# Performance work log

Measured on AMD Instinct MI355X. Metric: run time of the kernel, lower is better.

Reference implementation:

```python
import jax, jax.numpy as jnp
import numpy as np

B = 4096
D = 2048
K = 8          # num_intention
H2 = 64        # fc2 out


def setup_inputs() -> dict:
    key = jax.random.key(0)
    ks = jax.random.split(key, 8)
    x = jax.random.normal(ks[0], (B, D), dtype=jnp.float32)
    # one-hot intention per sample
    idx = jax.random.randint(ks[1], (B,), 0, K)
    intention = jax.nn.one_hot(idx, K, dtype=jnp.float32)
    s1 = 1.0 / np.sqrt(D)
    s2 = 1.0 / np.sqrt(K)
    s3 = 1.0 / np.sqrt(D + H2)
    W1 = jax.random.uniform(ks[2], (D * K, D), jnp.float32, -s1, s1)
    b1 = jax.random.uniform(ks[3], (D * K,), jnp.float32, -s1, s1)
    W2 = jax.random.uniform(ks[4], (H2, K), jnp.float32, -s2, s2)
    b2 = jax.random.uniform(ks[5], (H2,), jnp.float32, -s2, s2)
    W3 = jax.random.uniform(ks[6], (1, D + H2), jnp.float32, -s3, s3)
    b3 = jax.random.uniform(ks[7], (1,), jnp.float32, -s3, s3)
    return {"x": x, "intention": intention, "W1": W1, "b1": b1,
            "W2": W2, "b2": b2, "W3": W3, "b3": b3}


def reference(x, intention, W1, b1, W2, b2, W3, b3):
    # fc2 on the one-hot intention -> [B, 64]
    y2 = intention @ W2.T + b2
    # fc1 densely computes all K branches (dropout treated as identity / eval mode)
    y1 = x @ W1.T + b1                      # [B, D*K]
    # mask = intention.repeat(1, 2048): branch axis is INNERMOST (interleaved)
    y1 = y1.reshape(B, D, K)                # [B, D, K]
    sel = jax.lax.stop_gradient(intention)  # mask is non-differentiable in torch
    y1 = jnp.einsum('bdk,bk->bd', y1, sel)  # gather active branch -> [B, D]
    y3 = jax.nn.relu(jnp.concatenate([y1, y2], axis=1))  # [B, D+64]
    y = y3 @ W3.T + b3                      # [B, 1]
    return y
```

## Files before the change

### kernel.cpp

```cpp
#include <hip/hip_runtime.h>
#include <hip/hip_bf16.h>
#include <stdint.h>

#define NB 4096
#define ND 2048
#define NK 8
#define NH 64

#define BM 128
#define BN 128
#define BK 32
#define MAX_ROWS 5120
#define MAX_TILES 40

#define CONV_BLOCKS  (NK * ND)
#define XCONV_BLOCKS NB
#define KIDX_BLOCKS  (NB / 256)
#define PREP_GRID    (CONV_BLOCKS + XCONV_BLOCKS + KIDX_BLOCKS)

typedef __bf16 bf16;
typedef __bf16 bf16x8 __attribute__((ext_vector_type(8)));
typedef float floatx4 __attribute__((ext_vector_type(4)));

#define OFF_KIDX   0u
#define OFF_ORDER  16384u
#define OFF_META   40960u
#define OFF_CUR    41472u
#define OFF_C2S    41536u
#define OFF_CNTP   41600u
#define OFF_XC     65536u
#define OFF_WB     16842752u

__device__ inline void cvt_row16(const float* __restrict__ src, bf16* __restrict__ dst) {
    float4 a = *(const float4*)(src);
    float4 c = *(const float4*)(src + 4);
    bf16x8 v;
    v[0] = (bf16)a.x; v[1] = (bf16)a.y; v[2] = (bf16)a.z; v[3] = (bf16)a.w;
    v[4] = (bf16)c.x; v[5] = (bf16)c.y; v[6] = (bf16)c.z; v[7] = (bf16)c.w;
    *(bf16x8*)dst = v;
}

__global__ void __launch_bounds__(256)
prep_conv_kernel(const float* __restrict__ x,
                 const float* __restrict__ intention,
                 const float* __restrict__ W1,
                 int* __restrict__ kidx,
                 int* __restrict__ cntp,
                 bf16* __restrict__ xc,
                 bf16* __restrict__ Wb)
{
    const int blk = blockIdx.x;
    const int tid = threadIdx.x;

    if (blk < CONV_BLOCKS) {
        const int d = blk >> 3;
        const int k = blk & 7;
        cvt_row16(W1 + (size_t)blk * ND + tid * 8,
                  Wb + ((size_t)k * ND + d) * ND + tid * 8);
    } else if (blk < CONV_BLOCKS + XCONV_BLOCKS) {
        const int row = blk - CONV_BLOCKS;
        cvt_row16(x + (size_t)row * ND + tid * 8,
                  xc + (size_t)row * ND + tid * 8);
    } else {
        __shared__ int h[NK];
        const int hb = blk - CONV_BLOCKS - XCONV_BLOCKS;
        if (tid < NK) h[tid] = 0;
        __syncthreads();
        const int b = hb * 256 + tid;
        float4 a = *(const float4*)(intention + (size_t)b * NK);
        float4 c = *(const float4*)(intention + (size_t)b * NK + 4);
        int k = 0;
        if (a.y > 0.5f) k = 1;
        if (a.z > 0.5f) k = 2;
        if (a.w > 0.5f) k = 3;
        if (c.x > 0.5f) k = 4;
        if (c.y > 0.5f) k = 5;
        if (c.z > 0.5f) k = 6;
        if (c.w > 0.5f) k = 7;
        kidx[b] = k;
        atomicAdd(&h[k], 1);
        __syncthreads();
        if (tid < NK) cntp[hb * NK + tid] = h[tid];
    }
}

__global__ void __launch_bounds__(256)
meta_kernel(const int* __restrict__ cntp,
            const float* __restrict__ W2,
            const float* __restrict__ b2,
            const float* __restrict__ W3,
            const float* __restrict__ b3,
            int* __restrict__ meta,
            int* __restrict__ cursors,
            float* __restrict__ c2s)
{
    __shared__ int cnt[NK];
    const int tid = threadIdx.x;
    if (tid < NK) {
        int s = 0;
#pragma unroll
        for (int i = 0; i < KIDX_BLOCKS; i++) s += cntp[i * NK + tid];
        cnt[tid] = s;
    }
    if (tid >= 64 && tid < 128) {
        const int l = tid - 64;
        const int k = l & 7;
        const int hc = l >> 3;
        float s = 0.f;
#pragma unroll
        for (int j = 0; j < 8; j++) {
            int h = hc * 8 + j;
            float v = W2[h * NK + k] + b2[h];
            if (v > 0.f) s += v * W3[ND + h];
        }
        s += __shfl_xor(s, 8, 64);
        s += __shfl_xor(s, 16, 64);
        s += __shfl_xor(s, 32, 64);
        if (l < 8) c2s[k] = s + b3[0];
    }
    __syncthreads();
    if (tid == 0) {
        int running = 0, nt = 0;
        for (int k = 0; k < NK; k++) {
            cursors[k] = running;
            int ntile = (cnt[k] + BM - 1) / BM;
            for (int t = 0; t < ntile && nt < MAX_TILES; t++) {
                meta[1 + nt] = k;
                meta[1 + MAX_TILES + nt] = running + t * BM;
                nt++;
            }
            running += ntile * BM;
        }
        meta[0] = nt;
    }
}

__global__ void __launch_bounds__(256)
scatter_kernel(const int* __restrict__ kidx,
               int* __restrict__ cursors,
               const float* __restrict__ c2s,
               int* __restrict__ order,
               float* __restrict__ out)
{
    const int b = blockIdx.x * 256 + threadIdx.x;
    const int lane = threadIdx.x & 63;
    const int k = kidx[b] & 7;
    out[b] = c2s[k];

    const unsigned long long below = (lane == 63) ? ~0ull >> 1
                                   : ((1ull << lane) - 1);
    int pos = 0;
#pragma unroll
    for (int kk = 0; kk < NK; kk++) {
        unsigned long long m = __ballot(k == kk);
        if (m) {
            int leader = __ffsll((long long)m) - 1;
            int base = 0;
            if (lane == leader) base = atomicAdd(&cursors[kk], __popcll(m));
            base = __shfl(base, leader, 64);
            if (k == kk) pos = base + __popcll(m & below);
        }
    }
    if (pos >= 0 && pos < MAX_ROWS) order[pos] = b;
}

__global__ void __launch_bounds__(256)
gemm_kernel(const bf16* __restrict__ xc,
            const bf16* __restrict__ Wb,
            const int* __restrict__ order,
            const int* __restrict__ meta,
            const float* __restrict__ b1,
            const float* __restrict__ W3,
            float* __restrict__ out)
{
    int n_mt = meta[0];
    if (n_mt > MAX_TILES) n_mt = MAX_TILES;
    const int mt = blockIdx.y;
    if (mt >= n_mt) return;
    const int kbr = meta[1 + mt] & 7;
    int row0 = meta[1 + MAX_TILES + mt];
    if (row0 < 0) row0 = 0;
    if (row0 > MAX_ROWS - BM) row0 = MAX_ROWS - BM;
    const int col0 = blockIdx.x * BN;

    __shared__ bf16 As[BM * BK];
    __shared__ bf16 Bs[BN * BK];
    __shared__ int rowb[BM];

    const int tid = threadIdx.x;
    const int lane = tid & 63;
    const int wid = tid >> 6;
    const int wm = wid >> 1;
    const int wn = wid & 1;

    if (tid < BM) {
        int b = order[row0 + tid];
        rowb[tid] = (b >= 0 && b < NB) ? b : -1;
    }
    __syncthreads();

    const int srow = tid >> 2;
    const int scol = (tid & 3) * 8;
    const int ra0 = rowb[srow];
    const int ra1 = rowb[64 + srow];
    const bf16* pa0 = xc + (size_t)(ra0 < 0 ? 0 : ra0) * ND + scol;
    const bf16* pa1 = xc + (size_t)(ra1 < 0 ? 0 : ra1) * ND + scol;
    const bf16* pb0 = Wb + ((size_t)kbr * ND + col0 + srow) * ND + scol;
    const bf16* pb1 = pb0 + (size_t)64 * ND;
    bf16* la0 = As + wid * 512;
    bf16* la1 = As + 2048 + wid * 512;
    bf16* lb0 = Bs + wid * 512;
    bf16* lb1 = Bs + 2048 + wid * 512;

    floatx4 zero = {0.f, 0.f, 0.f, 0.f};
    floatx4 acc[4][4];
#pragma unroll
    for (int i = 0; i < 4; i++)
#pragma unroll
        for (int j = 0; j < 4; j++) acc[i][j] = zero;

    const int qk = (lane >> 4) * 8;
    const int mrow = lane & 15;

    for (int kk = 0; kk < ND; kk += BK) {
        __builtin_amdgcn_global_load_lds(
            (const __attribute__((address_space(1))) void*)(pa0 + kk),
            (__attribute__((address_space(3))) void*)la0, 16, 0, 0);
        __builtin_amdgcn_global_load_lds(
            (const __attribute__((address_space(1))) void*)(pa1 + kk),
            (__attribute__((address_space(3))) void*)la1, 16, 0, 0);
        __builtin_amdgcn_global_load_lds(
            (const __attribute__((address_space(1))) void*)(pb0 + kk),
            (__attribute__((address_space(3))) void*)lb0, 16, 0, 0);
        __builtin_amdgcn_global_load_lds(
            (const __attribute__((address_space(1))) void*)(pb1 + kk),
            (__attribute__((address_space(3))) void*)lb1, 16, 0, 0);
        __syncthreads();

        bf16x8 af[4], bfv[4];
#pragma unroll
        for (int i = 0; i < 4; i++) {
            af[i]  = *(const bf16x8*)(As + (wm * 64 + i * 16 + mrow) * BK + qk);
            bfv[i] = *(const bf16x8*)(Bs + (wn * 64 + i * 16 + mrow) * BK + qk);
        }
#pragma unroll
        for (int i = 0; i < 4; i++)
#pragma unroll
            for (int j = 0; j < 4; j++)
                acc[i][j] = __builtin_amdgcn_mfma_f32_16x16x32_bf16(
                    af[i], bfv[j], acc[i][j], 0, 0, 0);
        __syncthreads();
    }

    const int colq = lane & 15;
    const int quad = lane >> 4;
    float bias[4], w3v[4];
#pragma unroll
    for (int j = 0; j < 4; j++) {
        int d = col0 + wn * 64 + j * 16 + colq;
        bias[j] = b1[d * NK + kbr];
        w3v[j] = W3[d];
    }
#pragma unroll
    for (int i = 0; i < 4; i++) {
#pragma unroll
        for (int r = 0; r < 4; r++) {
            float s = 0.f;
#pragma unroll
            for (int j = 0; j < 4; j++) {
                float v = acc[i][j][r] + bias[j];
                s += (v > 0.f) ? v * w3v[j] : 0.f;
            }
#pragma unroll
            for (int m = 1; m < 16; m <<= 1) s += __shfl_xor(s, m, 64);
            if (colq == 0) {
                int b = rowb[wm * 64 + i * 16 + quad * 4 + r];
                if (b >= 0) atomicAdd(out + b, s);
            }
        }
    }
}

extern "C" void kernel_launch(void* const* d_in, const int* in_sizes, int n_in,
                              void* d_out, int out_size, void* d_ws, size_t ws_size,
                              hipStream_t stream)
{
    const float* x         = (const float*)d_in[0];
    const float* intention = (const float*)d_in[1];
    const float* W1        = (const float*)d_in[2];
    const float* b1        = (const float*)d_in[3];
    const float* W2        = (const float*)d_in[4];
    const float* b2        = (const float*)d_in[5];
    const float* W3        = (const float*)d_in[6];
    const float* b3        = (const float*)d_in[7];
    float* out = (float*)d_out;

    char* ws = (char*)d_ws;
    int*   kidx    = (int*)(ws + OFF_KIDX);
    int*   order   = (int*)(ws + OFF_ORDER);
    int*   meta    = (int*)(ws + OFF_META);
    int*   cursors = (int*)(ws + OFF_CUR);
    float* c2s     = (float*)(ws + OFF_C2S);
    int*   cntp    = (int*)(ws + OFF_CNTP);
    bf16*  xc      = (bf16*)(ws + OFF_XC);
    bf16*  Wb      = (bf16*)(ws + OFF_WB);

    prep_conv_kernel<<<dim3(PREP_GRID), dim3(256), 0, stream>>>(
        x, intention, W1, kidx, cntp, xc, Wb);
    meta_kernel<<<dim3(1), dim3(256), 0, stream>>>(
        cntp, W2, b2, W3, b3, meta, cursors, c2s);
    scatter_kernel<<<dim3(NB / 256), dim3(256), 0, stream>>>(
        kidx, cursors, c2s, order, out);
    gemm_kernel<<<dim3(ND / BN, MAX_TILES), dim3(256), 0, stream>>>(
        xc, Wb, order, meta, b1, W3, out);
}
```

Baseline: 312.1 us.

## Fold meta/scatter into prep block and widen GEMM to 512 threads with BK 64

Moves the intention histogram, branch-constant computation, tile metadata and row scatter into block 0 of the conversion kernel, removing two small kernel launches and their serialization. The GEMM now runs 8 waves per block, each owning a 64x32 output sub-tile, with a K step of 64 so there are half as many barrier-separated iterations. The single-block scatter uses shared-memory atomics, so row order inside each branch is no longer deterministic. Block 0 also does serial work that may finish after the conversion blocks.

```diff
diff --git a/kernel.cpp b/kernel.cpp
--- a/kernel.cpp
+++ b/kernel.cpp
@@ -9,25 +9,19 @@
 
 #define BM 128
 #define BN 128
-#define BK 32
+#define BK 64
 #define MAX_ROWS 5120
 #define MAX_TILES 40
 
-#define CONV_BLOCKS  (NK * ND)
-#define XCONV_BLOCKS NB
-#define KIDX_BLOCKS  (NB / 256)
-#define PREP_GRID    (CONV_BLOCKS + XCONV_BLOCKS + KIDX_BLOCKS)
+#define XCONV_FIRST (1 + NK * ND)
+#define PREP_GRID   (1 + NK * ND + NB)
 
 typedef __bf16 bf16;
 typedef __bf16 bf16x8 __attribute__((ext_vector_type(8)));
 typedef float floatx4 __attribute__((ext_vector_type(4)));
 
-#define OFF_KIDX   0u
-#define OFF_ORDER  16384u
-#define OFF_META   40960u
-#define OFF_CUR    41472u
-#define OFF_C2S    41536u
-#define OFF_CNTP   41600u
+#define OFF_ORDER  0u
+#define OFF_META   20480u
 #define OFF_XC     65536u
 #define OFF_WB     16842752u
 
@@ -41,130 +35,101 @@
 }
 
 __global__ void __launch_bounds__(256)
-prep_conv_kernel(const float* __restrict__ x,
+mega_prep_kernel(const float* __restrict__ x,
                  const float* __restrict__ intention,
                  const float* __restrict__ W1,
-                 int* __restrict__ kidx,
-                 int* __restrict__ cntp,
+                 const float* __restrict__ W2,
+                 const float* __restrict__ b2,
+                 const float* __restrict__ W3,
+                 const float* __restrict__ b3,
+                 int* __restrict__ order,
+                 int* __restrict__ meta,
                  bf16* __restrict__ xc,
-                 bf16* __restrict__ Wb)
+                 bf16* __restrict__ Wb,
+                 float* __restrict__ out)
 {
     const int blk = blockIdx.x;
     const int tid = threadIdx.x;
 
-    if (blk < CONV_BLOCKS) {
-        const int d = blk >> 3;
-        const int k = blk & 7;
-        cvt_row16(W1 + (size_t)blk * ND + tid * 8,
+    if (blk == 0) {
+        __shared__ int kk_s[NB];
+        __shared__ int cnt[NK];
+        __shared__ int cur[NK];
+        __shared__ float c2l[NK];
+
+        if (tid < NK) cnt[tid] = 0;
+        __syncthreads();
+
+        for (int b = tid; b < NB; b += 256) {
+            float4 a = *(const float4*)(intention + (size_t)b * NK);
+            float4 c = *(const float4*)(intention + (size_t)b * NK + 4);
+            int k = 0;
+            if (a.y > 0.5f) k = 1;
+            if (a.z > 0.5f) k = 2;
+            if (a.w > 0.5f) k = 3;
+            if (c.x > 0.5f) k = 4;
+            if (c.y > 0.5f) k = 5;
+            if (c.z > 0.5f) k = 6;
+            if (c.w > 0.5f) k = 7;
+            kk_s[b] = k;
+            atomicAdd(&cnt[k], 1);
+        }
+        __syncthreads();
+
+        if (tid < 64) {
+            const int k = tid & 7;
+            const int hc = tid >> 3;
+            float s = 0.f;
+#pragma unroll
+            for (int j = 0; j < 8; j++) {
+                int h = hc * 8 + j;
+                float v = W2[h * NK + k] + b2[h];
+                if (v > 0.f) s += v * W3[ND + h];
+            }
+            s += __shfl_xor(s, 8, 64);
+            s += __shfl_xor(s, 16, 64);
+            s += __shfl_xor(s, 32, 64);
+            if (tid < 8) c2l[k] = s + b3[0];
+        }
+        if (tid == 128) {
+            int running = 0, nt = 0;
+            int c[NK];
+#pragma unroll
+            for (int k = 0; k < NK; k++) c[k] = cnt[k];
+            for (int k = 0; k < NK; k++) {
+                cur[k] = running;
+                int ntile = (c[k] + BM - 1) / BM;
+                for (int t = 0; t < ntile && nt < MAX_TILES; t++) {
+                    meta[1 + nt] = k;
+                    meta[1 + MAX_TILES + nt] = running + t * BM;
+                    nt++;
+                }
+                running += ntile * BM;
+            }
+            meta[0] = nt;
+        }
+        __syncthreads();
+
+        for (int b = tid; b < NB; b += 256) {
+            int k = kk_s[b];
+            out[b] = c2l[k];
+            int pos = atomicAdd(&cur[k], 1);
+            if (pos >= 0 && pos < MAX_ROWS) order[pos] = b;
+        }
+    } else if (blk < XCONV_FIRST) {
+        const int r = blk - 1;
+        const int d = r >> 3;
+        const int k = r & 7;
+        cvt_row16(W1 + (size_t)r * ND + tid * 8,
                   Wb + ((size_t)k * ND + d) * ND + tid * 8);
-    } else if (blk < CONV_BLOCKS + XCONV_BLOCKS) {
-        const int row = blk - CONV_BLOCKS;
+    } else {
+        const int row = blk - XCONV_FIRST;
         cvt_row16(x + (size_t)row * ND + tid * 8,
                   xc + (size_t)row * ND + tid * 8);
-    } else {
-        __shared__ int h[NK];
-        const int hb = blk - CONV_BLOCKS - XCONV_BLOCKS;
-        if (tid < NK) h[tid] = 0;
-        __syncthreads();
-        const int b = hb * 256 + tid;
-        float4 a = *(const float4*)(intention + (size_t)b * NK);
-        float4 c = *(const float4*)(intention + (size_t)b * NK + 4);
-        int k = 0;
-        if (a.y > 0.5f) k = 1;
-        if (a.z > 0.5f) k = 2;
-        if (a.w > 0.5f) k = 3;
-        if (c.x > 0.5f) k = 4;
-        if (c.y > 0.5f) k = 5;
-        if (c.z > 0.5f) k = 6;
-        if (c.w > 0.5f) k = 7;
-        kidx[b] = k;
-        atomicAdd(&h[k], 1);
-        __syncthreads();
-        if (tid < NK) cntp[hb * NK + tid] = h[tid];
-    }
-}
-
-__global__ void __launch_bounds__(256)
-meta_kernel(const int* __restrict__ cntp,
-            const float* __restrict__ W2,
-            const float* __restrict__ b2,
-            const float* __restrict__ W3,
-            const float* __restrict__ b3,
-            int* __restrict__ meta,
-            int* __restrict__ cursors,
-            float* __restrict__ c2s)
-{
-    __shared__ int cnt[NK];
-    const int tid = threadIdx.x;
-    if (tid < NK) {
-        int s = 0;
-#pragma unroll
-        for (int i = 0; i < KIDX_BLOCKS; i++) s += cntp[i * NK + tid];
-        cnt[tid] = s;
-    }
-    if (tid >= 64 && tid < 128) {
-        const int l = tid - 64;
-        const int k = l & 7;
-        const int hc = l >> 3;
-        float s = 0.f;
-#pragma unroll
-        for (int j = 0; j < 8; j++) {
-            int h = hc * 8 + j;
-            float v = W2[h * NK + k] + b2[h];
-            if (v > 0.f) s += v * W3[ND + h];
-        }
-        s += __shfl_xor(s, 8, 64);
-        s += __shfl_xor(s, 16, 64);
-        s += __shfl_xor(s, 32, 64);
-        if (l < 8) c2s[k] = s + b3[0];
-    }
-    __syncthreads();
-    if (tid == 0) {
-        int running = 0, nt = 0;
-        for (int k = 0; k < NK; k++) {
-            cursors[k] = running;
-            int ntile = (cnt[k] + BM - 1) / BM;
-            for (int t = 0; t < ntile && nt < MAX_TILES; t++) {
-                meta[1 + nt] = k;
-                meta[1 + MAX_TILES + nt] = running + t * BM;
-                nt++;
-            }
-            running += ntile * BM;
-        }
-        meta[0] = nt;
-    }
-}
-
-__global__ void __launch_bounds__(256)
-scatter_kernel(const int* __restrict__ kidx,
-               int* __restrict__ cursors,
-               const float* __restrict__ c2s,
-               int* __restrict__ order,
-               float* __restrict__ out)
-{
-    const int b = blockIdx.x * 256 + threadIdx.x;
-    const int lane = threadIdx.x & 63;
-    const int k = kidx[b] & 7;
-    out[b] = c2s[k];
-
-    const unsigned long long below = (lane == 63) ? ~0ull >> 1
-                                   : ((1ull << lane) - 1);
-    int pos = 0;
-#pragma unroll
-    for (int kk = 0; kk < NK; kk++) {
-        unsigned long long m = __ballot(k == kk);
-        if (m) {
-            int leader = __ffsll((long long)m) - 1;
-            int base = 0;
-            if (lane == leader) base = atomicAdd(&cursors[kk], __popcll(m));
-            base = __shfl(base, leader, 64);
-            if (k == kk) pos = base + __popcll(m & below);
-        }
-    }
-    if (pos >= 0 && pos < MAX_ROWS) order[pos] = b;
-}
-
-__global__ void __launch_bounds__(256)
+    }
+}
+
+__global__ void __launch_bounds__(512, 4)
 gemm_kernel(const bf16* __restrict__ xc,
             const bf16* __restrict__ Wb,
             const int* __restrict__ order,
@@ -189,9 +154,9 @@
 
     const int tid = threadIdx.x;
     const int lane = tid & 63;
-    const int wid = tid >> 6;
-    const int wm = wid >> 1;
-    const int wn = wid & 1;
+    const int w = tid >> 6;
+    const int wm = w & 1;
+    const int wn = w >> 1;
 
     if (tid < BM) {
         int b = order[row0 + tid];
@@ -199,25 +164,25 @@
     }
     __syncthreads();
 
-    const int srow = tid >> 2;
-    const int scol = (tid & 3) * 8;
-    const int ra0 = rowb[srow];
-    const int ra1 = rowb[64 + srow];
-    const bf16* pa0 = xc + (size_t)(ra0 < 0 ? 0 : ra0) * ND + scol;
-    const bf16* pa1 = xc + (size_t)(ra1 < 0 ? 0 : ra1) * ND + scol;
-    const bf16* pb0 = Wb + ((size_t)kbr * ND + col0 + srow) * ND + scol;
-    const bf16* pb1 = pb0 + (size_t)64 * ND;
-    bf16* la0 = As + wid * 512;
-    bf16* la1 = As + 2048 + wid * 512;
-    bf16* lb0 = Bs + wid * 512;
-    bf16* lb1 = Bs + 2048 + wid * 512;
+    const int sr0 = w * 16 + (lane >> 3);
+    const int sc = (lane & 7) * 8;
+    const int ra0 = rowb[sr0];
+    const int ra1 = rowb[sr0 + 8];
+    const bf16* pa0 = xc + (size_t)(ra0 < 0 ? 0 : ra0) * ND + sc;
+    const bf16* pa1 = xc + (size_t)(ra1 < 0 ? 0 : ra1) * ND + sc;
+    const bf16* pb0 = Wb + ((size_t)kbr * ND + col0 + sr0) * ND + sc;
+    const bf16* pb1 = pb0 + (size_t)8 * ND;
+    bf16* la0 = As + w * 1024;
+    bf16* la1 = As + w * 1024 + 512;
+    bf16* lb0 = Bs + w * 1024;
+    bf16* lb1 = Bs + w * 1024 + 512;
 
     floatx4 zero = {0.f, 0.f, 0.f, 0.f};
-    floatx4 acc[4][4];
+    floatx4 acc[4][2];
 #pragma unroll
     for (int i = 0; i < 4; i++)
 #pragma unroll
-        for (int j = 0; j < 4; j++) acc[i][j] = zero;
+        for (int j = 0; j < 2; j++) acc[i][j] = zero;
 
     const int qk = (lane >> 4) * 8;
     const int mrow = lane & 15;
@@ -237,27 +202,34 @@
             (__attribute__((address_space(3))) void*)lb1, 16, 0, 0);
         __syncthreads();
 
-        bf16x8 af[4], bfv[4];
-#pragma unroll
-        for (int i = 0; i < 4; i++) {
-            af[i]  = *(const bf16x8*)(As + (wm * 64 + i * 16 + mrow) * BK + qk);
-            bfv[i] = *(const bf16x8*)(Bs + (wn * 64 + i * 16 + mrow) * BK + qk);
-        }
+        bf16x8 af[4][2], bfv[2][2];
 #pragma unroll
         for (int i = 0; i < 4; i++)
 #pragma unroll
-            for (int j = 0; j < 4; j++)
-                acc[i][j] = __builtin_amdgcn_mfma_f32_16x16x32_bf16(
-                    af[i], bfv[j], acc[i][j], 0, 0, 0);
+            for (int t = 0; t < 2; t++)
+                af[i][t] = *(const bf16x8*)(As + (wm * 64 + i * 16 + mrow) * BK + t * 32 + qk);
+#pragma unroll
+        for (int j = 0; j < 2; j++)
+#pragma unroll
+            for (int t = 0; t < 2; t++)
+                bfv[j][t] = *(const bf16x8*)(Bs + (wn * 32 + j * 16 + mrow) * BK + t * 32 + qk);
+#pragma unroll
+        for (int t = 0; t < 2; t++)
+#pragma unroll
+            for (int i = 0; i < 4; i++)
+#pragma unroll
+                for (int j = 0; j < 2; j++)
+                    acc[i][j] = __builtin_amdgcn_mfma_f32_16x16x32_bf16(
+                        af[i][t], bfv[j][t], acc[i][j], 0, 0, 0);
         __syncthreads();
     }
 
     const int colq = lane & 15;
     const int quad = lane >> 4;
-    float bias[4], w3v[4];
-#pragma unroll
-    for (int j = 0; j < 4; j++) {
-        int d = col0 + wn * 64 + j * 16 + colq;
+    float bias[2], w3v[2];
+#pragma unroll
+    for (int j = 0; j < 2; j++) {
+        int d = col0 + wn * 32 + j * 16 + colq;
         bias[j] = b1[d * NK + kbr];
         w3v[j] = W3[d];
     }
@@ -267,7 +239,7 @@
         for (int r = 0; r < 4; r++) {
             float s = 0.f;
 #pragma unroll
-            for (int j = 0; j < 4; j++) {
+            for (int j = 0; j < 2; j++) {
                 float v = acc[i][j][r] + bias[j];
                 s += (v > 0.f) ? v * w3v[j] : 0.f;
             }
@@ -296,21 +268,13 @@
     float* out = (float*)d_out;
 
     char* ws = (char*)d_ws;
-    int*   kidx    = (int*)(ws + OFF_KIDX);
-    int*   order   = (int*)(ws + OFF_ORDER);
-    int*   meta    = (int*)(ws + OFF_META);
-    int*   cursors = (int*)(ws + OFF_CUR);
-    float* c2s     = (float*)(ws + OFF_C2S);
-    int*   cntp    = (int*)(ws + OFF_CNTP);
-    bf16*  xc      = (bf16*)(ws + OFF_XC);
-    bf16*  Wb      = (bf16*)(ws + OFF_WB);
-
-    prep_conv_kernel<<<dim3(PREP_GRID), dim3(256), 0, stream>>>(
-        x, intention, W1, kidx, cntp, xc, Wb);
-    meta_kernel<<<dim3(1), dim3(256), 0, stream>>>(
-        cntp, W2, b2, W3, b3, meta, cursors, c2s);
-    scatter_kernel<<<dim3(NB / 256), dim3(256), 0, stream>>>(
-        kidx, cursors, c2s, order, out);
-    gemm_kernel<<<dim3(ND / BN, MAX_TILES), dim3(256), 0, stream>>>(
+    int*   order = (int*)(ws + OFF_ORDER);
+    int*   meta  = (int*)(ws + OFF_META);
+    bf16*  xc    = (bf16*)(ws + OFF_XC);
+    bf16*  Wb    = (bf16*)(ws + OFF_WB);
+
+    mega_prep_kernel<<<dim3(PREP_GRID), dim3(256), 0, stream>>>(
+        x, intention, W1, W2, b2, W3, b3, order, meta, xc, Wb, out);
+    gemm_kernel<<<dim3(ND / BN, MAX_TILES), dim3(512), 0, stream>>>(
         xc, Wb, order, meta, b1, W3, out);
 }
```

After: 358.4 us. 1.15x slower.
